# Kernel tuning notes

Hardware: AMD Instinct MI355X
Metric: run time of the kernel (lower is better)

The kernel has to match this reference:

```python
import jax, jax.numpy as jnp
import numpy as np

B, N, C = 4, 4096, 256
GROUPS = 50
M_SCALE = 10.0


def setup_inputs() -> dict:
    key = jax.random.key(0)
    ks = jax.random.split(key, 6)
    s = 0.02
    return {
        "inputs": jax.random.normal(ks[0], (B, N, 1, C), dtype=jnp.float32),
        "W_sem": jax.random.normal(ks[1], (C, 128), dtype=jnp.float32) * s,
        "b_sem": jnp.zeros((128,), jnp.float32),
        "W_seg": jax.random.normal(ks[2], (128, GROUPS), dtype=jnp.float32) * s,
        "b_seg": jnp.zeros((GROUPS,), jnp.float32),
        "W_sim": jax.random.normal(ks[3], (C, 128), dtype=jnp.float32) * s,
        "b_sim": jnp.zeros((128,), jnp.float32),
        "W_conf": jax.random.normal(ks[4], (C, 128), dtype=jnp.float32) * s,
        "b_conf": jnp.zeros((128,), jnp.float32),
        "W_cl": jax.random.normal(ks[5], (128, 1), dtype=jnp.float32) * s,
        "b_cl": jnp.zeros((1,), jnp.float32),
    }


def reference(inputs, W_sem, b_sem, W_seg, b_seg, W_sim, b_sim,
              W_conf, b_conf, W_cl, b_cl):
    # 1x1 Conv2D on [B, N, 1, C] == per-point dense layer on channels.
    x = inputs[:, :, 0, :]  # [B, N, C]

    # Semantic segmentation head
    Fsem = jnp.einsum('bnc,cd->bnd', x, W_sem) + b_sem          # [B, N, 128]
    ptssemseg_logits = jnp.einsum('bnd,dg->bng', Fsem, W_seg) + b_seg  # [B, N, G]
    ptssemseg = jax.nn.softmax(ptssemseg_logits, axis=-1)

    # Similarity head: pairwise squared distances of Fsim rows
    Fsim = jnp.einsum('bnc,cd->bnd', x, W_sim) + b_sim          # [B, N, 128]
    r = jnp.sum(Fsim * Fsim, axis=2)                             # [B, N]
    gram = jnp.einsum('bnd,bmd->bnm', Fsim, Fsim)                # [B, N, N]
    D = r[:, :, None] - 2.0 * gram + r[:, None, :]               # [B, N, N]
    simmat_logits = jnp.maximum(M_SCALE * D, 0.0)

    # Confidence head
    Fconf = jnp.einsum('bnc,cd->bnd', x, W_conf) + b_conf        # [B, N, 128]
    conf_logits = jnp.einsum('bnd,do->bno', Fconf, W_cl) + b_cl  # [B, N, 1]
    conf = jax.nn.sigmoid(conf_logits)

    return (ptssemseg, ptssemseg_logits, simmat_logits, conf, conf_logits)
```

## Files before the change

kernel.cpp:

```cpp
#include <hip/hip_runtime.h>
#include <cstdint>
#include <cstddef>

#define NN 4096
#define CC 256
#define GG 50
#define PB 32
#define JD 384

#define O_OUT1 819200
#define O_OUT2 1638400
#define O_OUT3 68747264
#define O_OUT4 68763648

__device__ __forceinline__ unsigned bf16b(float f) {
    unsigned u = __float_as_uint(f);
    return (u + 0x7FFFu + ((u >> 16) & 1u)) >> 16;
}
__device__ __forceinline__ float bf16f(short s) {
    return __uint_as_float(((unsigned)(unsigned short)s) << 16);
}

__global__ __launch_bounds__(256) void k_proj(
    const float* __restrict__ x,
    const float* __restrict__ Wsem, const float* __restrict__ bsem,
    const float* __restrict__ Wseg, const float* __restrict__ bseg,
    const float* __restrict__ Wsim, const float* __restrict__ bsim,
    const float* __restrict__ Wconf, const float* __restrict__ bconf,
    const float* __restrict__ Wcl, const float* __restrict__ bcl,
    unsigned* __restrict__ fsimu,
    float* __restrict__ out0, float* __restrict__ out1,
    float* __restrict__ out3, float* __restrict__ out4)
{
    __shared__ float smem[15360];
    __shared__ float confl[PB], mxs[PB], sms[PB];

    float* xs  = smem;
    float* wch = smem + 9216;

    int t = threadIdx.x;
    int pbase = blockIdx.x * PB;
    if (t < PB) confl[t] = 0.f;

    #pragma unroll 4
    for (int p = 0; p < PB; ++p)
        xs[t * 36 + p] = x[(size_t)(pbase + p) * CC + t];

    int tj = t & 31, tp = t >> 5;
    float acc[4][12];
    #pragma unroll
    for (int pp = 0; pp < 4; ++pp)
        #pragma unroll
        for (int jj = 0; jj < 12; ++jj) acc[pp][jj] = 0.f;

    for (int kc = 0; kc < 16; ++kc) {
        __syncthreads();
        #pragma unroll
        for (int i = 0; i < 8; ++i) {
            int idx = i * 256 + t;
            int k = idx >> 7, jj = idx & 127;
            int g = (kc * 16 + k) * 128 + jj;
            wch[k * JD +       jj] = Wsim[g];
            wch[k * JD + 128 + jj] = Wsem[g];
            wch[k * JD + 256 + jj] = Wconf[g];
        }
        __syncthreads();
        #pragma unroll
        for (int k = 0; k < 16; ++k) {
            const float* xp = &xs[(kc * 16 + k) * 36 + tp * 4];
            float a0 = xp[0], a1 = xp[1], a2 = xp[2], a3 = xp[3];
            const float* wr = &wch[k * JD + tj * 12];
            #pragma unroll
            for (int jj = 0; jj < 12; ++jj) {
                float w = wr[jj];
                acc[0][jj] = fmaf(a0, w, acc[0][jj]);
                acc[1][jj] = fmaf(a1, w, acc[1][jj]);
                acc[2][jj] = fmaf(a2, w, acc[2][jj]);
                acc[3][jj] = fmaf(a3, w, acc[3][jj]);
            }
        }
    }
    __syncthreads();

    float* hsem = smem;
    float* WsT  = smem + 4224;
    float* segl = smem + 10824;

    for (int i = t; i < GG * 128; i += 256) {
        int g = i >> 7, d = i & 127;
        WsT[g * 132 + d] = Wseg[d * GG + g];
    }

    #pragma unroll
    for (int pp = 0; pp < 4; ++pp) {
        int p = tp * 4 + pp;
        float vv[12];
        #pragma unroll
        for (int jj = 0; jj < 12; ++jj) {
            int j = tj * 12 + jj;
            float bb = (j < 128) ? bsim[j] : (j < 256 ? bsem[j - 128] : bconf[j - 256]);
            vv[jj] = acc[pp][jj] + bb;
        }
        #pragma unroll
        for (int jj = 0; jj < 12; jj += 2) {
            int j = tj * 12 + jj;
            if (j < 128)
                fsimu[(size_t)(pbase + p) * 64 + (j >> 1)] =
                    bf16b(vv[jj]) | (bf16b(vv[jj + 1]) << 16);
        }
        #pragma unroll
        for (int jj = 0; jj < 12; ++jj) {
            int j = tj * 12 + jj;
            if (j >= 128 && j < 256) hsem[p * 132 + (j - 128)] = vv[jj];
        }
        float c = 0.f;
        #pragma unroll
        for (int jj = 0; jj < 12; ++jj) {
            int j = tj * 12 + jj;
            if (j >= 256) c = fmaf(vv[jj], Wcl[j - 256], c);
        }
        if (tj >= 21) atomicAdd(&confl[p], c);
    }
    __syncthreads();

    for (int i = t; i < PB * GG; i += 256) {
        int p = i / GG, g = i - p * GG;
        const float4* hp = (const float4*)&hsem[p * 132];
        const float4* wp = (const float4*)&WsT[g * 132];
        float a = bseg[g];
        #pragma unroll 8
        for (int d = 0; d < 32; ++d) {
            float4 h = hp[d], w = wp[d];
            a = fmaf(h.x, w.x, a); a = fmaf(h.y, w.y, a);
            a = fmaf(h.z, w.z, a); a = fmaf(h.w, w.w, a);
        }
        segl[p * 52 + g] = a;
    }
    __syncthreads();

    if (t < PB) {
        int p = t;
        float mx = -1e30f;
        for (int g = 0; g < GG; ++g) mx = fmaxf(mx, segl[p * 52 + g]);
        float s = 0.f;
        for (int g = 0; g < GG; ++g) s += __expf(segl[p * 52 + g] - mx);
        mxs[p] = mx; sms[p] = 1.f / s;
        float cl = confl[p] + bcl[0];
        out4[pbase + p] = cl;
        out3[pbase + p] = 1.f / (1.f + __expf(-cl));
    }
    __syncthreads();

    for (int i = t; i < PB * GG; i += 256) {
        int p = i / GG, g = i - p * GG;
        float l = segl[p * 52 + g];
        size_t o = (size_t)(pbase + p) * GG + g;
        out1[o] = l;
        out0[o] = __expf(l - mxs[p]) * sms[p];
    }
}

typedef short short8 __attribute__((ext_vector_type(8)));
typedef float f32x4 __attribute__((ext_vector_type(4)));

__global__ __launch_bounds__(256) void k_simmat(
    const short* __restrict__ fs, float* __restrict__ out2)
{
    int t = threadIdx.x;
    int lane = t & 63, wv = t >> 6;
    int b = blockIdx.z;
    int J = blockIdx.x * 128 + (wv & 1) * 64;
    int I = blockIdx.y * 128 + (wv >> 1) * 64;
    int rowl = lane & 15, quad = lane >> 4;

    const short8* F = (const short8*)(fs + (size_t)b * NN * 128);

    f32x4 acc[4][4];
    #pragma unroll
    for (int r = 0; r < 4; ++r)
        #pragma unroll
        for (int c = 0; c < 4; ++c) { f32x4 z = {0.f,0.f,0.f,0.f}; acc[r][c] = z; }
    float sra[4] = {0.f,0.f,0.f,0.f}, srb[4] = {0.f,0.f,0.f,0.f};

    #pragma unroll
    for (int s = 0; s < 4; ++s) {
        short8 av[4], bv[4];
        #pragma unroll
        for (int r = 0; r < 4; ++r)
            av[r] = F[(size_t)(I + r * 16 + rowl) * 16 + s * 4 + quad];
        #pragma unroll
        for (int c = 0; c < 4; ++c)
            bv[c] = F[(size_t)(J + c * 16 + rowl) * 16 + s * 4 + quad];
        #pragma unroll
        for (int r = 0; r < 4; ++r)
            #pragma unroll
            for (int e = 0; e < 8; ++e) {
                float f = bf16f(av[r][e]); sra[r] = fmaf(f, f, sra[r]);
            }
        #pragma unroll
        for (int c = 0; c < 4; ++c)
            #pragma unroll
            for (int e = 0; e < 8; ++e) {
                float f = bf16f(bv[c][e]); srb[c] = fmaf(f, f, srb[c]);
            }
        #pragma unroll
        for (int r = 0; r < 4; ++r)
            #pragma unroll
            for (int c = 0; c < 4; ++c)
                acc[r][c] = __builtin_amdgcn_mfma_f32_16x16x32_bf16(av[r], bv[c], acc[r][c], 0, 0, 0);
    }

    #pragma unroll
    for (int r = 0; r < 4; ++r) {
        sra[r] += __shfl_xor(sra[r], 16);
        sra[r] += __shfl_xor(sra[r], 32);
    }
    #pragma unroll
    for (int c = 0; c < 4; ++c) {
        srb[c] += __shfl_xor(srb[c], 16);
        srb[c] += __shfl_xor(srb[c], 32);
    }
    float riq[4][4];
    #pragma unroll
    for (int r = 0; r < 4; ++r)
        #pragma unroll
        for (int e = 0; e < 4; ++e)
            riq[r][e] = __shfl(sra[r], quad * 4 + e);

    float* ob = out2 + (size_t)b * NN * NN;
    #pragma unroll
    for (int r = 0; r < 4; ++r) {
        int rbase = I + r * 16 + quad * 4;
        #pragma unroll
        for (int c = 0; c < 4; ++c) {
            int col = J + c * 16 + rowl;
            float rj = srb[c];
            f32x4 v = acc[r][c];
            #pragma unroll
            for (int e = 0; e < 4; ++e) {
                float dv = 10.f * (riq[r][e] + rj) - 20.f * v[e];
                ob[(size_t)(rbase + e) * NN + col] = fmaxf(dv, 0.f);
            }
        }
    }
}

extern "C" void kernel_launch(void* const* d_in, const int* in_sizes, int n_in,
                              void* d_out, int out_size, void* d_ws, size_t ws_size,
                              hipStream_t stream)
{
    const float* x     = (const float*)d_in[0];
    const float* Wsem  = (const float*)d_in[1];
    const float* bsem  = (const float*)d_in[2];
    const float* Wseg  = (const float*)d_in[3];
    const float* bseg  = (const float*)d_in[4];
    const float* Wsim  = (const float*)d_in[5];
    const float* bsim  = (const float*)d_in[6];
    const float* Wconf = (const float*)d_in[7];
    const float* bconf = (const float*)d_in[8];
    const float* Wcl   = (const float*)d_in[9];
    const float* bcl   = (const float*)d_in[10];

    if (ws_size < (size_t)4 * NN * 128 * 2) return;
    unsigned* fsim = (unsigned*)d_ws;

    float* out  = (float*)d_out;
    float* out0 = out;
    float* out1 = out + O_OUT1;
    float* out2 = out + O_OUT2;
    float* out3 = out + O_OUT3;
    float* out4 = out + O_OUT4;

    hipLaunchKernelGGL(k_proj, dim3(512), dim3(256), 0, stream,
                       x, Wsem, bsem, Wseg, bseg, Wsim, bsim, Wconf, bconf, Wcl, bcl,
                       fsim, out0, out1, out3, out4);
    hipLaunchKernelGGL(k_simmat, dim3(32, 32, 4), dim3(256), 0, stream,
                       (const short*)fsim, out2);
}
```

Before: 422.7 us.

## Exploit simmat symmetry, precompute row norms, use nontemporal stores

The simmat kernel now launches only upper-triangular 128x128 tiles (528 per batch) and writes each computed tile both directly and transposed, halving the MFMA and Fsim load work. Squared row norms are computed once in the projection kernel from the bf16-rounded values, using a shared-memory atomic reduction, and stored to workspace instead of being recomputed per tile. Output stores become nontemporal. The transposed writes are float4 stores along rows of the mirrored tile, so write coalescing differs from the direct writes. The kernel is dominated by the 256MB output write, so the benefit is bounded by bandwidth.

After: 422.7 us. No clear change (+0.0%).

```diff
diff --git a/kernel.cpp b/kernel.cpp
--- a/kernel.cpp
+++ b/kernel.cpp
@@ -28,19 +28,19 @@
     const float* __restrict__ Wsim, const float* __restrict__ bsim,
     const float* __restrict__ Wconf, const float* __restrict__ bconf,
     const float* __restrict__ Wcl, const float* __restrict__ bcl,
-    unsigned* __restrict__ fsimu,
+    unsigned* __restrict__ fsimu, float* __restrict__ rnorm,
     float* __restrict__ out0, float* __restrict__ out1,
     float* __restrict__ out3, float* __restrict__ out4)
 {
     __shared__ float smem[15360];
-    __shared__ float confl[PB], mxs[PB], sms[PB];
+    __shared__ float confl[PB], mxs[PB], sms[PB], rns[PB];
 
     float* xs  = smem;
     float* wch = smem + 9216;
 
     int t = threadIdx.x;
     int pbase = blockIdx.x * PB;
-    if (t < PB) confl[t] = 0.f;
+    if (t < PB) { confl[t] = 0.f; rns[t] = 0.f; }
 
     #pragma unroll 4
     for (int p = 0; p < PB; ++p)
@@ -101,6 +101,16 @@
             float bb = (j < 128) ? bsim[j] : (j < 256 ? bsem[j - 128] : bconf[j - 256]);
             vv[jj] = acc[pp][jj] + bb;
         }
+        float rsq = 0.f;
+        #pragma unroll
+        for (int jj = 0; jj < 12; ++jj) {
+            int j = tj * 12 + jj;
+            if (j < 128) {
+                float f = bf16f((short)bf16b(vv[jj]));
+                rsq = fmaf(f, f, rsq);
+            }
+        }
+        if (tj <= 10) atomicAdd(&rns[p], rsq);
         #pragma unroll
         for (int jj = 0; jj < 12; jj += 2) {
             int j = tj * 12 + jj;
@@ -148,6 +158,7 @@
         float cl = confl[p] + bcl[0];
         out4[pbase + p] = cl;
         out3[pbase + p] = 1.f / (1.f + __expf(-cl));
+        rnorm[pbase + p] = rns[p];
     }
     __syncthreads();
 
@@ -164,23 +175,30 @@
 typedef float f32x4 __attribute__((ext_vector_type(4)));
 
 __global__ __launch_bounds__(256) void k_simmat(
-    const short* __restrict__ fs, float* __restrict__ out2)
+    const short* __restrict__ fs, const float* __restrict__ rn, float* __restrict__ out2)
 {
     int t = threadIdx.x;
     int lane = t & 63, wv = t >> 6;
-    int b = blockIdx.z;
-    int J = blockIdx.x * 128 + (wv & 1) * 64;
-    int I = blockIdx.y * 128 + (wv >> 1) * 64;
+    int b = blockIdx.y;
+
+    int p = blockIdx.x;
+    int tj = (int)((sqrtf((float)(8 * p + 1)) - 1.f) * 0.5f);
+    while ((tj + 1) * (tj + 2) / 2 <= p) ++tj;
+    while (tj * (tj + 1) / 2 > p) --tj;
+    int ti = p - tj * (tj + 1) / 2;
+
+    int I = ti * 128 + (wv >> 1) * 64;
+    int J = tj * 128 + (wv & 1) * 64;
     int rowl = lane & 15, quad = lane >> 4;
 
     const short8* F = (const short8*)(fs + (size_t)b * NN * 128);
+    const float* rb = rn + b * NN;
 
     f32x4 acc[4][4];
     #pragma unroll
     for (int r = 0; r < 4; ++r)
         #pragma unroll
         for (int c = 0; c < 4; ++c) { f32x4 z = {0.f,0.f,0.f,0.f}; acc[r][c] = z; }
-    float sra[4] = {0.f,0.f,0.f,0.f}, srb[4] = {0.f,0.f,0.f,0.f};
 
     #pragma unroll
     for (int s = 0; s < 4; ++s) {
@@ -194,53 +212,55 @@
         #pragma unroll
         for (int r = 0; r < 4; ++r)
             #pragma unroll
-            for (int e = 0; e < 8; ++e) {
-                float f = bf16f(av[r][e]); sra[r] = fmaf(f, f, sra[r]);
-            }
-        #pragma unroll
-        for (int c = 0; c < 4; ++c)
-            #pragma unroll
-            for (int e = 0; e < 8; ++e) {
-                float f = bf16f(bv[c][e]); srb[c] = fmaf(f, f, srb[c]);
-            }
-        #pragma unroll
-        for (int r = 0; r < 4; ++r)
-            #pragma unroll
             for (int c = 0; c < 4; ++c)
                 acc[r][c] = __builtin_amdgcn_mfma_f32_16x16x32_bf16(av[r], bv[c], acc[r][c], 0, 0, 0);
     }
 
-    #pragma unroll
-    for (int r = 0; r < 4; ++r) {
-        sra[r] += __shfl_xor(sra[r], 16);
-        sra[r] += __shfl_xor(sra[r], 32);
-    }
-    #pragma unroll
-    for (int c = 0; c < 4; ++c) {
-        srb[c] += __shfl_xor(srb[c], 16);
-        srb[c] += __shfl_xor(srb[c], 32);
-    }
-    float riq[4][4];
+    f32x4 rI4[4];
+    float rJs[4];
     #pragma unroll
     for (int r = 0; r < 4; ++r)
-        #pragma unroll
-        for (int e = 0; e < 4; ++e)
-            riq[r][e] = __shfl(sra[r], quad * 4 + e);
+        rI4[r] = *(const f32x4*)&rb[I + r * 16 + quad * 4];
+    #pragma unroll
+    for (int c = 0; c < 4; ++c)
+        rJs[c] = rb[J + c * 16 + rowl];
+
+    #pragma unroll
+    for (int r = 0; r < 4; ++r)
+        #pragma unroll
+        for (int c = 0; c < 4; ++c) {
+            f32x4 v = acc[r][c];
+            float rj = rJs[c];
+            f32x4 o;
+            #pragma unroll
+            for (int e = 0; e < 4; ++e)
+                o[e] = fmaxf(10.f * (rI4[r][e] + rj) - 20.f * v[e], 0.f);
+            acc[r][c] = o;
+        }
 
     float* ob = out2 + (size_t)b * NN * NN;
+
     #pragma unroll
     for (int r = 0; r < 4; ++r) {
         int rbase = I + r * 16 + quad * 4;
         #pragma unroll
         for (int c = 0; c < 4; ++c) {
             int col = J + c * 16 + rowl;
-            float rj = srb[c];
             f32x4 v = acc[r][c];
             #pragma unroll
-            for (int e = 0; e < 4; ++e) {
-                float dv = 10.f * (riq[r][e] + rj) - 20.f * v[e];
-                ob[(size_t)(rbase + e) * NN + col] = fmaxf(dv, 0.f);
-            }
+            for (int e = 0; e < 4; ++e)
+                __builtin_nontemporal_store(v[e], &ob[(size_t)(rbase + e) * NN + col]);
+        }
+    }
+
+    if (ti != tj) {
+        #pragma unroll
+        for (int c = 0; c < 4; ++c) {
+            size_t rowoff = (size_t)(J + c * 16 + rowl) * NN;
+            #pragma unroll
+            for (int r = 0; r < 4; ++r)
+                __builtin_nontemporal_store(acc[r][c],
+                    (f32x4*)&ob[rowoff + (I + r * 16 + quad * 4)]);
         }
     }
 }
@@ -261,8 +281,10 @@
     const float* Wcl   = (const float*)d_in[9];
     const float* bcl   = (const float*)d_in[10];
 
-    if (ws_size < (size_t)4 * NN * 128 * 2) return;
+    const size_t FSIM_BYTES = (size_t)4 * NN * 128 * 2;
+    if (ws_size < FSIM_BYTES + (size_t)4 * NN * sizeof(float)) return;
     unsigned* fsim = (unsigned*)d_ws;
+    float* rnorm = (float*)((char*)d_ws + FSIM_BYTES);
 
     float* out  = (float*)d_out;
     float* out0 = out;
@@ -273,7 +295,7 @@
 
     hipLaunchKernelGGL(k_proj, dim3(512), dim3(256), 0, stream,
                        x, Wsem, bsem, Wseg, bseg, Wsim, bsim, Wconf, bconf, Wcl, bcl,
-                       fsim, out0, out1, out3, out4);
-    hipLaunchKernelGGL(k_simmat, dim3(32, 32, 4), dim3(256), 0, stream,
-                       (const short*)fsim, out2);
-}
+                       fsim, rnorm, out0, out1, out3, out4);
+    hipLaunchKernelGGL(k_simmat, dim3(528, 4, 1), dim3(256), 0, stream,
+                       (const short*)fsim, rnorm, out2);
+}
```
